# Performance work log

Hardware: AMD Instinct MI355X
Metric: run time of the kernel (lower is better)

The kernel has to match this reference:

```python
import jax, jax.numpy as jnp
import numpy as np
from jax import lax

BLOCK = 64      # block_size
OVERLAP = 16
NITER = 64      # Niter init kwarg; loop runs min(1000, Niter)
L = 0.24        # diffusion step size
K = 0.03        # exp(logk), logk = log(0.03)
DEPS = 0.1
FFT_STEPS = 10
THRESH = 0.1    # uniform-region variance threshold


def _g(x):
    # g(x) = 1 / (1 + |x^2| / K^2)
    return 1.0 / (1.0 + jnp.abs(x * x) / (K * K))


def _avgpool3(x):
    # F.avg_pool2d(x, 3, stride=1, padding=1) with count_include_pad=True (divide by 9)
    s = lax.reduce_window(x, 0.0, lax.add, (1, 1, 3, 3), (1, 1, 1, 1),
                          [(0, 0), (0, 0), (1, 1), (1, 1)])
    return s / 9.0


def _fft_diffuse_block(block, bcv, bch):
    cv_mean = bcv.mean()
    ch_mean = bch.mean()
    h, w = block.shape[2], block.shape[3]
    ky = jnp.arange(h, dtype=block.dtype)[:, None] * (2.0 * np.pi / h)      # [h,1]
    kx = jnp.arange(w // 2 + 1, dtype=block.dtype)[None, :] * (2.0 * np.pi / w)  # [1,w//2+1]
    op = (1.0 - 2.0 * L * (cv_mean * (1.0 - jnp.cos(ky)) + ch_mean * (1.0 - jnp.cos(kx)))) ** FFT_STEPS
    return jnp.fft.irfft2(jnp.fft.rfft2(block) * op, s=(h, w))


def _forward(guide, initial):
    # depth shift for stability (torch code branches on initial.min() <= deps)
    shift = jnp.where(initial.min() <= DEPS, DEPS, 0.0).astype(initial.dtype)
    depth = initial + shift

    # diffusion coefficients from guide: cv [B,1,H-1,W], ch [B,1,H,W-1]
    cv = _g(jnp.mean(jnp.abs(guide[:, :, 1:, :] - guide[:, :, :-1, :]), axis=1, keepdims=True))
    ch = _g(jnp.mean(jnp.abs(guide[:, :, :, 1:] - guide[:, :, :, :-1]), axis=1, keepdims=True))

    # identify_uniform_regions (local variance via avg pools); original torch code
    # broadcasts shapes (H-1,W) & (H,W-1) which errors -- we crop to common (H-1,W-1)
    cv_var = _avgpool3(cv ** 2) - _avgpool3(cv) ** 2
    ch_var = _avgpool3(ch ** 2) - _avgpool3(ch) ** 2
    uniform = ((cv_var[:, :, :, :-1] < THRESH) & (ch_var[:, :, :-1, :] < THRESH)).astype(depth.dtype)

    B, C, H, W = depth.shape
    step = BLOCK - OVERLAP
    # sequential per-block FFT diffusion with overlap blending (blocks read
    # depth updated by previous blocks, so order matters)
    for b in range(B):
        for y in range(0, H, step):
            for x in range(0, W, step):
                y_end = min(y + BLOCK, H)
                x_end = min(x + BLOCK, W)
                bh, bw = y_end - y, x_end - x
                block = depth[b:b + 1, :, y:y_end, x:x_end]
                bcv = cv[b:b + 1, :, y:y_end - 1, x:x_end]
                bch = ch[b:b + 1, :, y:y_end, x:x_end - 1]
                bun = uniform[b:b + 1, :, y:y_end, x:x_end]  # clips at edges (H-1,W-1)
                cond = bun.mean() > 0.7
                newb = _fft_diffuse_block(block, bcv, bch)
                if y > 0 or x > 0:
                    blend_y = jnp.ones((bh,), depth.dtype)
                    if y > 0:
                        r = jnp.arange(bh)
                        blend_y = jnp.where(r < min(OVERLAP, bh), r.astype(depth.dtype) / OVERLAP, blend_y)
                    blend_x = jnp.ones((bw,), depth.dtype)
                    if x > 0:
                        r = jnp.arange(bw)
                        blend_x = jnp.where(r < min(OVERLAP, bw), r.astype(depth.dtype) / OVERLAP, blend_x)
                    blend = (blend_y[:, None] * blend_x[None, :])[None, None]
                    cand = block * (1.0 - blend) + newb * blend
                else:
                    cand = newb
                region = jnp.where(cond, cand, block)
                depth = depth.at[b:b + 1, :, y:y_end, x:x_end].set(region)

    # explicit anisotropic diffusion stencil, serial data dependence -> lax.scan
    def diffuse_step(I, _):
        dv = I[:, :, 1:, :] - I[:, :, :-1, :]
        dh = I[:, :, :, 1:] - I[:, :, :, :-1]  # computed before vertical update (as in torch)
        tv = L * cv * dv
        I = I.at[:, :, 1:, :].add(-tv).at[:, :, :-1, :].add(tv)
        th = L * ch * dh
        I = I.at[:, :, :, 1:].add(-th).at[:, :, :, :-1].add(th)
        return I, None

    depth, _ = lax.scan(diffuse_step, depth, None, length=min(1000, NITER))
    y_pred = depth - shift
    return y_pred, cv, ch


def setup_inputs() -> dict:
    key = jax.random.key(0)
    k1, k2 = jax.random.split(key)
    guide = jax.random.uniform(k1, (2, 3, 512, 512), dtype=jnp.float32)
    initial = jax.random.uniform(k2, (2, 1, 512, 512), dtype=jnp.float32)
    return {"guide": guide, "initial": initial}


def reference(guide, initial):
    # returns (y_pred, cv, ch) matching {'y_pred':..., 'cv':..., 'ch':...}
    return _forward(guide, initial)
```

## Files before the change

### kernel.cpp

```cpp
#include <hip/hip_runtime.h>
#include <stdint.h>

#define LDIFF 0.24f

constexpr int H = 512, W = 512, NB = 2;
constexpr int HW = H * W;
constexpr int N_D = NB * HW;
constexpr int CVH = 511, CVW = 512;
constexpr int CHH = 512, CHW = 511;
constexpr int N_CV = NB * CVH * CVW;
constexpr int NBLKS = 11;
constexpr int NBT = NB * 121;

__device__ inline float ldc(const float* p) {
    return __hip_atomic_load(p, __ATOMIC_RELAXED, __HIP_MEMORY_SCOPE_AGENT);
}
__device__ inline void stc(float* p, float v) {
    __hip_atomic_store(p, v, __ATOMIC_RELAXED, __HIP_MEMORY_SCOPE_AGENT);
}
__device__ inline int ldci(const int* p) {
    return __hip_atomic_load(p, __ATOMIC_RELAXED, __HIP_MEMORY_SCOPE_AGENT);
}
__device__ inline void stci(int* p, int v) {
    __hip_atomic_store(p, v, __ATOMIC_RELAXED, __HIP_MEMORY_SCOPE_AGENT);
}

__device__ inline float rot_a(float x) {
    return __int_as_float(__builtin_amdgcn_update_dpp(0, __float_as_int(x), 0x134, 0xf, 0xf, false));
}
__device__ inline float rot_b(float x) {
    return __int_as_float(__builtin_amdgcn_update_dpp(0, __float_as_int(x), 0x13c, 0xf, 0xf, false));
}
__device__ inline float sh_a(float x) {
    return __int_as_float(__builtin_amdgcn_update_dpp(0, __float_as_int(x), 0x130, 0xf, 0xf, true));
}
__device__ inline float sh_b(float x) {
    return __int_as_float(__builtin_amdgcn_update_dpp(0, __float_as_int(x), 0x138, 0xf, 0xf, true));
}

#define BSTEP(SRC, DST, LO, HI)                                                   \
    _Pragma("unroll")                                                             \
    for (int m = (LO); m <= (HI); m++) {                                          \
        float hs = rot_a(SRC[m]) + rot_b(SRC[m]);                                 \
        DST[m] = SRC[m] + a * (SRC[m - 1] + SRC[m + 1] - 2.0f * SRC[m])           \
                        + bc * (hs - 2.0f * SRC[m]);                              \
    }

#define CSTEP(SRC, DST, LO, HI)                                                   \
    _Pragma("unroll")                                                             \
    for (int m = (LO); m <= (HI); m++) {                                          \
        float Vm = SRC[m] + LDIFF * cve[m] * (SRC[m + 1] - SRC[m])                \
                          - LDIFF * cve[m - 1] * (SRC[m] - SRC[m - 1]);           \
        float rA = rot_a(Vm), rB = rot_b(Vm);                                     \
        float lf = dirL ? rA : rB, rt = dirL ? rB : rA;                           \
        DST[m] = Vm + LDIFF * che[m] * (rt - Vm) - LDIFF * chle[m] * (Vm - lf);   \
    }

__global__ __launch_bounds__(256) void kall(
    const float* __restrict__ guide, const float* __restrict__ initial,
    float* __restrict__ cv, float* __restrict__ ch,
    float* __restrict__ D, float* __restrict__ T0, float* __restrict__ T1,
    float* __restrict__ ypred, int* __restrict__ sync_)
{
    __shared__ float cvT[73 * 74];
    __shared__ float chT[73 * 74];
    __shared__ float xT[2][4][5][64];
    __shared__ float xB[2][4][5][64];
    __shared__ float red[12];
    __shared__ float prmS[3];

    int* wflag = sync_;
    int* dflag = sync_ + 16384;

    const int blk = blockIdx.x;
    const int i = blk / NBLKS, j = blk % NBLKS;
    const int b = blockIdx.y;
    const int tid = threadIdx.x;
    const int lane = tid & 63, wv = tid >> 6;
    const int r0 = wv * 16;
    const int me = b * 121 + blk;

    const int y0 = i * 48, x0 = j * 48;
    const int y1 = min(y0 + 64, 512), x1 = min(x0 + 64, 512);
    const int bh = y1 - y0, bw = x1 - x0;
    const int yb = y0 - 8, xb = x0 - 8;
    const float kinv = 1.0f / (0.03f * 0.03f);

    const float* gb = guide + (size_t)b * 3 * HW;
    for (int p = tid; p < 73 * 73; p += 256) {
        int rr = p / 73, cc2 = p - rr * 73;
        int y = yb + rr, x = xb + cc2;
        float cvv = 0.0f, chv = 0.0f;
        if (y >= 0 && y < 512 && x >= 0 && x < 512) {
            const float* g = gb + y * W + x;
            float g0 = g[0], g1 = g[HW], g2 = g[2 * HW];
            if (y < 511) {
                float d = (fabsf(g[W] - g0) + fabsf(g[HW + W] - g1) + fabsf(g[2 * HW + W] - g2)) * (1.0f / 3.0f);
                cvv = 1.0f / (1.0f + d * d * kinv);
            }
            if (x < 511) {
                float d = (fabsf(g[1] - g0) + fabsf(g[HW + 1] - g1) + fabsf(g[2 * HW + 1] - g2)) * (1.0f / 3.0f);
                chv = 1.0f / (1.0f + d * d * kinv);
            }
        }
        cvT[rr * 74 + cc2] = cvv;
        chT[rr * 74 + cc2] = chv;
    }
    __syncthreads();

    {
        int rcv = min(y0 + 48, CVH) - y0, ccv = min(x0 + 48, CVW) - x0;
        float* cvo = cv + b * CVH * CVW;
        for (int p = tid; p < rcv * ccv; p += 256) {
            int r = p / ccv, c = p - r * ccv;
            cvo[(y0 + r) * CVW + x0 + c] = cvT[(r + 8) * 74 + c + 8];
        }
        int rch = min(y0 + 48, CHH) - y0, cch = min(x0 + 48, CHW) - x0;
        float* cho = ch + b * CHH * CHW;
        for (int p = tid; p < rch * cch; p += 256) {
            int r = p / cch, c = p - r * cch;
            cho[(y0 + r) * CHW + x0 + c] = chT[(r + 8) * 74 + c + 8];
        }
    }

    float scv = 0.f, sch = 0.f, sun = 0.f;
    {
        int n = (bh - 1) * bw;
        for (int p = tid; p < n; p += 256) { int r = p / bw, c = p - r * bw; scv += cvT[(r + 8) * 74 + c + 8]; }
    }
    {
        int cols = bw - 1, n = bh * cols;
        for (int p = tid; p < n; p += 256) { int r = p / cols, c = p - r * cols; sch += chT[(r + 8) * 74 + c + 8]; }
    }
    const int ur = min(y1, 511) - y0, uc = min(x1, 511) - x0;
    {
        int n = ur * uc;
        for (int p = tid; p < n; p += 256) {
            int r = p / uc, c = p - r * uc;
            float s1 = 0.f, s2 = 0.f, t1 = 0.f, t2 = 0.f;
            #pragma unroll
            for (int dy = 0; dy < 3; dy++)
                #pragma unroll
                for (int dx = 0; dx < 3; dx++) {
                    float v = cvT[(r + 7 + dy) * 74 + c + 7 + dx]; s1 += v; s2 += v * v;
                    float w2 = chT[(r + 7 + dy) * 74 + c + 7 + dx]; t1 += w2; t2 += w2 * w2;
                }
            float m = s1 * (1.0f / 9.0f);
            float vcv = s2 * (1.0f / 9.0f) - m * m;
            m = t1 * (1.0f / 9.0f);
            float vch = t2 * (1.0f / 9.0f) - m * m;
            if (vcv < 0.1f && vch < 0.1f) sun += 1.f;
        }
    }
    #pragma unroll
    for (int m = 1; m < 64; m <<= 1) {
        scv += __shfl_xor(scv, m);
        sch += __shfl_xor(sch, m);
        sun += __shfl_xor(sun, m);
    }
    if (lane == 0) { red[wv * 3] = scv; red[wv * 3 + 1] = sch; red[wv * 3 + 2] = sun; }
    __syncthreads();
    if (tid == 0) {
        float a0 = red[0] + red[3] + red[6] + red[9];
        float a1 = red[1] + red[4] + red[7] + red[10];
        float a2 = red[2] + red[5] + red[8] + red[11];
        prmS[0] = a0 / (float)((bh - 1) * bw);
        prmS[1] = a1 / (float)(bh * (bw - 1));
        prmS[2] = (a2 / (float)(ur * uc) > 0.7f) ? 1.0f : 0.0f;
    }
    __syncthreads();

    int prb = __builtin_amdgcn_update_dpp(0, lane, 0x134, 0xf, 0xf, false);
    const bool dirL = (prb == ((lane + 63) & 63));

    const bool cond = prmS[2] > 0.5f;
    const float a = LDIFF * prmS[0], bc = LDIFF * prmS[1];
    float* Db = D + b * HW;
    const float* ini = initial + b * HW;

    const int mh = bh - 1, mw = bw - 1;
    const int ccw = lane & mw;

    if (!cond) {
        #pragma unroll
        for (int k = 0; k < 16; k++) {
            int r = r0 + k;
            if (r < bh && (i == 0 || r >= 16) && lane < bw && (j == 0 || lane >= 16)) {
                int ad = (y0 + r) * W + x0 + lane;
                stc(&Db[ad], ini[ad]);
            }
        }
        asm volatile("s_waitcnt vmcnt(0)" ::: "memory");
        if (lane == 0) {
            stci(&wflag[me * 64 + wv * 16], 1);
            stci(&wflag[me * 64 + wv * 16 + 8], 1);
        }
    } else {
        float u[16], orig[16];
        int addr[16]; bool fD[16];
        #pragma unroll
        for (int k = 0; k < 16; k++) {
            int rr = (r0 + k) & mh;
            addr[k] = (y0 + rr) * W + x0 + ccw;
            fD[k] = (i > 0 && rr < 16) || (j > 0 && ccw < 16);
            if (!fD[k]) orig[k] = ini[addr[k]];
        }
        {
            const int Lw = (r0 & mh) >> 4;
            const bool needU = (i > 0) && ((r0 & mh) < 16);
            bool need = false;
            const int* fp = &wflag[me * 64];
            if (lane == 0) {
                if (j > 0) { need = true; fp = &wflag[(me - 1) * 64 + Lw * 16]; }
            } else if (lane == 1) {
                if (needU) { need = true; fp = &wflag[(me - NBLKS) * 64 + 3 * 16]; }
            } else if (lane == 2) {
                if (needU && j < 10) { need = true; fp = &wflag[(me - NBLKS + 1) * 64 + 3 * 16]; }
            } else if (lane == 3) {
                if (needU && j > 0) { need = true; fp = &wflag[(me - NBLKS - 1) * 64 + 3 * 16]; }
            }
            while (true) {
                int v = need ? ldci(fp) : 1;
                if (__ballot(v == 0) == 0) break;
                __builtin_amdgcn_s_sleep(0);
            }
        }
        #pragma unroll
        for (int k = 0; k < 16; k++) if (fD[k]) orig[k] = ldc(&Db[addr[k]]);
        #pragma unroll
        for (int k = 0; k < 16; k++) u[k] = orig[k];

        float wa[26], wb[26];
        #pragma unroll
        for (int g = 0; g < 2; ++g) {
            #pragma unroll
            for (int q = 0; q < 5; q++) {
                xT[g][wv][q][lane] = u[q];
                xB[g][wv][q][lane] = u[11 + q];
            }
            __syncthreads();
            #pragma unroll
            for (int q = 0; q < 5; q++) {
                wa[q]      = xB[g][(wv + 3) & 3][q][lane];
                wa[21 + q] = xT[g][(wv + 1) & 3][q][lane];
            }
            #pragma unroll
            for (int q = 0; q < 16; q++) wa[5 + q] = u[q];
            BSTEP(wa, wb, 1, 24);
            BSTEP(wb, wa, 2, 23);
            BSTEP(wa, wb, 3, 22);
            BSTEP(wb, wa, 4, 21);
            BSTEP(wa, wb, 5, 20);
            #pragma unroll
            for (int q = 0; q < 16; q++) u[q] = wb[5 + q];
        }

        #pragma unroll
        for (int k = 0; k < 16; k++) {
            int r = r0 + k;
            float byw = (y0 > 0 && r < 16) ? (float)r * (1.0f / 16.0f) : 1.0f;
            float bxw = (x0 > 0 && lane < 16) ? (float)lane * (1.0f / 16.0f) : 1.0f;
            float wgt = byw * bxw;
            u[k] = orig[k] * (1.0f - wgt) + u[k] * wgt;
        }
        #pragma unroll
        for (int k = 0; k < 16; k++) {
            int r = r0 + k;
            bool in = (r < bh && lane < bw);
            bool sc = (bw == 64 && lane >= 48) || (r >= 48);
            if (in && sc) stc(&Db[(y0 + r) * W + x0 + lane], u[k]);
        }
        asm volatile("s_waitcnt vmcnt(0)" ::: "memory");
        if (lane == 0) stci(&wflag[me * 64 + wv * 16], 1);
        #pragma unroll
        for (int k = 0; k < 16; k++) {
            int r = r0 + k;
            bool in = (r < bh && lane < bw);
            bool sc = (bw == 64 && lane >= 48) || (r >= 48);
            if (in && !sc) stc(&Db[(y0 + r) * W + x0 + lane], u[k]);
        }
        asm volatile("s_waitcnt vmcnt(0)" ::: "memory");
        if (lane == 0) stci(&wflag[me * 64 + wv * 16 + 8], 1);
    }
    __syncthreads();

    const int cx = xb + lane;
    const int gxc = min(max(cx, 0), 511);
    int gyA[16];
    #pragma unroll
    for (int k = 0; k < 16; k++) {
        int cy = yb + r0 + k;
        gyA[k] = min(max(cy, 0), 511);
    }
    float cve[24], che[24], chle[24];
    #pragma unroll
    for (int m = 0; m < 24; m++) {
        int rr = r0 + m - 4;
        bool ok = (rr >= 0);
        cve[m] = ok ? cvT[rr * 74 + lane] : 0.0f;
        che[m] = ok ? chT[rr * 74 + lane] : 0.0f;
        chle[m] = dirL ? sh_a(che[m]) : sh_b(che[m]);
    }

    float* Tb0 = T0 + b * HW;
    float* Tb1 = T1 + b * HW;
    float* ypb = ypred + b * HW;

    const int coreh = min(48, 512 - y0), corew = min(48, 512 - x0);
    const bool laneC = (lane >= 8) && (lane < 8 + corew);
    bool ownc[16], ringk[16];
    #pragma unroll
    for (int k = 0; k < 16; k++) {
        int wr = r0 + k;
        ownc[k] = laneC && (wr >= 8) && (wr < 8 + coreh);
        int cr = wr - 8, cl = lane - 8;
        ringk[k] = ownc[k] && (cr < 8 || cr >= coreh - 8 || cl < 8 || cl >= corew - 8);
    }

    float u[16];
    for (int t = 1; t <= 8; t++) {
        if (wv == 0) {
            bool need = false;
            const int* fp = &wflag[me * 64];
            int thr = 1;
            if (t == 1) {
                if (lane < 36) {
                    int nb = lane >> 2;
                    int di = nb / 3 - 1, dj = nb % 3 - 1;
                    int ni = i + di, nj = j + dj;
                    if ((di | dj) != 0 && ni >= 0 && ni < NBLKS && nj >= 0 && nj < NBLKS) {
                        need = true;
                        fp = &wflag[(b * 121 + ni * NBLKS + nj) * 64 + (lane & 3) * 16 + 8];
                    }
                }
            } else {
                thr = t - 1;
                if (lane < 9) {
                    int di = lane / 3 - 1, dj = lane % 3 - 1;
                    int ni = i + di, nj = j + dj;
                    if ((di | dj) != 0 && ni >= 0 && ni < NBLKS && nj >= 0 && nj < NBLKS) {
                        need = true;
                        fp = &dflag[(b * 121 + ni * NBLKS + nj) * 16];
                    }
                }
            }
            while (true) {
                int v = need ? ldci(fp) : 0x7fffffff;
                if (__ballot(v < thr) == 0) break;
                __builtin_amdgcn_s_sleep(8);
            }
        }
        __syncthreads();
        const float* src = (t == 1) ? Db : (((t - 1) & 1) ? Tb1 : Tb0);
        if (t == 1) {
            #pragma unroll
            for (int k = 0; k < 16; k++) u[k] = ldc(&src[gyA[k] * W + gxc]);
        } else {
            #pragma unroll
            for (int k = 0; k < 16; k++) if (!ownc[k]) u[k] = ldc(&src[gyA[k] * W + gxc]);
        }

        #pragma unroll
        for (int g = 0; g < 2; ++g) {
            #pragma unroll
            for (int q = 0; q < 4; q++) {
                xT[g][wv][q][lane] = u[q];
                xB[g][wv][q][lane] = u[12 + q];
            }
            __syncthreads();
            float wa[24], wb[24];
            #pragma unroll
            for (int q = 0; q < 4; q++) {
                wa[q]      = (wv > 0) ? xB[g][wv - 1][q][lane] : u[0];
                wa[20 + q] = (wv < 3) ? xT[g][wv + 1][q][lane] : u[15];
            }
            #pragma unroll
            for (int q = 0; q < 16; q++) wa[4 + q] = u[q];
            CSTEP(wa, wb, 1, 22);
            CSTEP(wb, wa, 2, 21);
            CSTEP(wa, wb, 3, 20);
            CSTEP(wb, wa, 4, 19);
            #pragma unroll
            for (int q = 0; q < 16; q++) u[q] = wa[4 + q];
        }

        if (t < 8) {
            float* dst = (t & 1) ? Tb1 : Tb0;
            #pragma unroll
            for (int k = 0; k < 16; k++) {
                if (ringk[k]) stc(&dst[(yb + r0 + k) * W + xb + lane], u[k]);
            }
            asm volatile("s_waitcnt vmcnt(0)" ::: "memory");
            __syncthreads();
            if (tid == 0) stci(&dflag[me * 16], t);
        } else {
            #pragma unroll
            for (int k = 0; k < 16; k++) {
                if (ownc[k]) ypb[(yb + r0 + k) * W + xb + lane] = u[k];
            }
        }
    }
}

extern "C" void kernel_launch(void* const* d_in, const int* in_sizes, int n_in,
                              void* d_out, int out_size, void* d_ws, size_t ws_size,
                              hipStream_t stream) {
    const float* guide   = (const float*)d_in[0];
    const float* initial = (const float*)d_in[1];
    float* y_pred = (float*)d_out;
    float* cv = y_pred + N_D;
    float* ch = cv + N_CV;

    uint8_t* w = (uint8_t*)d_ws;
    int* sync_ = (int*)w;
    float* D  = (float*)(w + 131072);
    float* T0 = (float*)(w + 131072 + (size_t)N_D * 4);
    float* T1 = (float*)(w + 131072 + (size_t)2 * N_D * 4);

    (void)hipMemsetAsync(sync_, 0, 131072, stream);
    kall<<<dim3(121, NB), 256, 0, stream>>>(guide, initial, cv, ch, D, T0, T1, y_pred, sync_);
}
```

Measured before the change: 307.0 us.

## Replace per-launch memset with double-buffered self-resetting sync flags

Measured after the change: 285.4 us. 1.08x faster.

```diff
diff --git a/kernel.cpp b/kernel.cpp
--- a/kernel.cpp
+++ b/kernel.cpp
@@ -2,6 +2,7 @@
 #include <stdint.h>
 
 #define LDIFF 0.24f
+#define MAGIC 0x5EED0B0B
 
 constexpr int H = 512, W = 512, NB = 2;
 constexpr int HW = H * W;
@@ -42,18 +43,17 @@
     _Pragma("unroll")                                                             \
     for (int m = (LO); m <= (HI); m++) {                                          \
         float hs = rot_a(SRC[m]) + rot_b(SRC[m]);                                 \
-        DST[m] = SRC[m] + a * (SRC[m - 1] + SRC[m + 1] - 2.0f * SRC[m])           \
-                        + bc * (hs - 2.0f * SRC[m]);                              \
+        float vs = SRC[m - 1] + SRC[m + 1];                                       \
+        DST[m] = fmaf(a, vs, fmaf(bc, hs, c0 * SRC[m]));                          \
     }
 
 #define CSTEP(SRC, DST, LO, HI)                                                   \
     _Pragma("unroll")                                                             \
     for (int m = (LO); m <= (HI); m++) {                                          \
-        float Vm = SRC[m] + LDIFF * cve[m] * (SRC[m + 1] - SRC[m])                \
-                          - LDIFF * cve[m - 1] * (SRC[m] - SRC[m - 1]);           \
+        float Vm = SRC[m] + cve[m] * (SRC[m + 1] - SRC[m])                        \
+                          - cve[m - 1] * (SRC[m] - SRC[m - 1]);                   \
         float rA = rot_a(Vm), rB = rot_b(Vm);                                     \
-        float lf = dirL ? rA : rB, rt = dirL ? rB : rA;                           \
-        DST[m] = Vm + LDIFF * che[m] * (rt - Vm) - LDIFF * chle[m] * (Vm - lf);   \
+        DST[m] = Vm + Pq[m] * (rB - Vm) - Qq[m] * (Vm - rA);                      \
     }
 
 __global__ __launch_bounds__(256) void kall(
@@ -68,9 +68,7 @@
     __shared__ float xB[2][4][5][64];
     __shared__ float red[12];
     __shared__ float prmS[3];
-
-    int* wflag = sync_;
-    int* dflag = sync_ + 16384;
+    __shared__ int ctlS[2];
 
     const int blk = blockIdx.x;
     const int i = blk / NBLKS, j = blk % NBLKS;
@@ -79,6 +77,29 @@
     const int lane = tid & 63, wv = tid >> 6;
     const int r0 = wv * 16;
     const int me = b * 121 + blk;
+
+    if (tid == 0) {
+        int mg = ldci(&sync_[65536]);
+        int pw = ldci(&sync_[65537]);
+        ctlS[0] = (mg == MAGIC) ? 1 : 0;
+        ctlS[1] = (mg == MAGIC) ? (pw & 1) : 0;
+    }
+    __syncthreads();
+    const int havemg = ctlS[0], par = ctlS[1];
+    int* wflag = sync_ + par * 32768;
+    int* dflag = wflag + 16384;
+    {
+        int* oth = sync_ + (par ^ 1) * 32768;
+        if (tid < 64) stci(&oth[me * 64 + tid], 0);
+        if (tid < 16) stci(&oth[16384 + me * 16 + tid], 0);
+        if (!havemg) {
+            if (tid < 64) stci(&wflag[me * 64 + tid], 0);
+            if (tid < 16) stci(&dflag[me * 16 + tid], 0);
+            if (me == 0 && tid == 0) { stci(&sync_[65537], 0); stci(&sync_[65538], 0); }
+        }
+        asm volatile("s_waitcnt vmcnt(0)" ::: "memory");
+    }
+    __syncthreads();
 
     const int y0 = i * 48, x0 = j * 48;
     const int y1 = min(y0 + 64, 512), x1 = min(x0 + 64, 512);
@@ -175,6 +196,7 @@
 
     const bool cond = prmS[2] > 0.5f;
     const float a = LDIFF * prmS[0], bc = LDIFF * prmS[1];
+    const float c0 = 1.0f - 2.0f * a - 2.0f * bc;
     float* Db = D + b * HW;
     const float* ini = initial + b * HW;
 
@@ -292,14 +314,17 @@
         int cy = yb + r0 + k;
         gyA[k] = min(max(cy, 0), 511);
     }
-    float cve[24], che[24], chle[24];
+    float cve[24], Pq[24], Qq[24];
     #pragma unroll
     for (int m = 0; m < 24; m++) {
         int rr = r0 + m - 4;
         bool ok = (rr >= 0);
-        cve[m] = ok ? cvT[rr * 74 + lane] : 0.0f;
-        che[m] = ok ? chT[rr * 74 + lane] : 0.0f;
-        chle[m] = dirL ? sh_a(che[m]) : sh_b(che[m]);
+        float cvv = ok ? cvT[rr * 74 + lane] : 0.0f;
+        float chh = ok ? chT[rr * 74 + lane] : 0.0f;
+        float chl = dirL ? sh_a(chh) : sh_b(chh);
+        cve[m] = LDIFF * cvv;
+        Pq[m] = LDIFF * (dirL ? chh : chl);
+        Qq[m] = LDIFF * (dirL ? chl : chh);
     }
 
     float* Tb0 = T0 + b * HW;
@@ -347,7 +372,7 @@
             while (true) {
                 int v = need ? ldci(fp) : 0x7fffffff;
                 if (__ballot(v < thr) == 0) break;
-                __builtin_amdgcn_s_sleep(8);
+                __builtin_amdgcn_s_sleep(4);
             }
         }
         __syncthreads();
@@ -398,6 +423,16 @@
             for (int k = 0; k < 16; k++) {
                 if (ownc[k]) ypb[(yb + r0 + k) * W + xb + lane] = u[k];
             }
+        }
+    }
+
+    __syncthreads();
+    if (tid == 0) {
+        int n = __hip_atomic_fetch_add(&sync_[65538], 1, __ATOMIC_RELAXED, __HIP_MEMORY_SCOPE_AGENT);
+        if (n == NBT - 1) {
+            stci(&sync_[65538], 0);
+            stci(&sync_[65537], par ^ 1);
+            stci(&sync_[65536], MAGIC);
         }
     }
 }
@@ -413,10 +448,9 @@
 
     uint8_t* w = (uint8_t*)d_ws;
     int* sync_ = (int*)w;
-    float* D  = (float*)(w + 131072);
-    float* T0 = (float*)(w + 131072 + (size_t)N_D * 4);
-    float* T1 = (float*)(w + 131072 + (size_t)2 * N_D * 4);
-
-    (void)hipMemsetAsync(sync_, 0, 131072, stream);
+    float* D  = (float*)(w + 262656);
+    float* T0 = D + N_D;
+    float* T1 = T0 + N_D;
+
     kall<<<dim3(121, NB), 256, 0, stream>>>(guide, initial, cv, ch, D, T0, T1, y_pred, sync_);
 }
```
